# Kernel optimization log

Measured on AMD Instinct MI355X. Metric: run time of the kernel, lower is better.

The kernel has to match this reference:

```python
import jax, jax.numpy as jnp
import numpy as np

B, S, K, N = 4, 2048, 4096, 4096
GS = 128
G = K // GS  # 32 groups


def setup_inputs() -> dict:
    key = jax.random.key(0)
    k1, k2, k3, k4, k5 = jax.random.split(key, 5)
    x = jax.random.normal(k1, (B, S, K), dtype=jnp.float16)
    # packed 4-bit weights: 8 nibbles per int32 along K
    qweight = jax.random.randint(k2, (K // 8, N), 0, 2**31 - 1, dtype=jnp.int32)
    # packed 4-bit zeros: 8 nibbles per int32 along N
    qzeros = jax.random.randint(k3, (G, N // 8), 0, 2**31 - 1, dtype=jnp.int32)
    scales = (jax.random.uniform(k4, (G, N), dtype=jnp.float32) * 0.009 + 0.001).astype(jnp.float16)
    g_idx = (jnp.arange(K, dtype=jnp.int32) // GS).astype(jnp.int32)
    bias = (jax.random.normal(k5, (N,), dtype=jnp.float32) * 0.01).astype(jnp.float16)
    return {"x": x, "qweight": qweight, "qzeros": qzeros, "scales": scales,
            "g_idx": g_idx, "bias": bias}


def _dequantize(qweight, qzeros, scales, g_idx):
    """GPTQ/ExLlama int4 grouped dequant -> fp16 weight [K, N]."""
    shifts = jnp.arange(8, dtype=jnp.int32) * 4
    # unpack qweight along K: [K/8, N] -> [K/8, 8, N] -> [K, N]
    q = ((qweight[:, None, :] >> shifts[None, :, None]) & 0xF).reshape(-1, qweight.shape[1])
    # unpack qzeros along N: [G, N/8] -> [G, N/8, 8] -> [G, N]; GPTQ stores z-1
    z = (((qzeros[:, :, None] >> shifts[None, None, :]) & 0xF).reshape(qzeros.shape[0], -1) + 1)
    zr = z[g_idx]          # [K, N] via per-row group gather (act-order general form)
    sr = scales[g_idx]     # [K, N]
    return (q.astype(sr.dtype) - zr.astype(sr.dtype)) * sr


def reference(x, qweight, qzeros, scales, g_idx, bias):
    W = _dequantize(qweight, qzeros, scales, g_idx)  # [K, N] fp16
    xf = x.reshape(-1, x.shape[-1])                  # [B*S, K]
    out = jnp.matmul(xf, W, preferred_element_type=jnp.float32).astype(x.dtype)
    out = out.reshape(x.shape[:-1] + (W.shape[1],)) + bias
    return out
```

## Files before the change

### kernel.cpp

```cpp
#include <hip/hip_runtime.h>

typedef __attribute__((ext_vector_type(8))) _Float16 halfx8;
typedef __attribute__((ext_vector_type(8))) short short8;
typedef __attribute__((ext_vector_type(4))) float f32x4;

#define DI __device__ __forceinline__

DI unsigned short h2us(_Float16 h) { return __builtin_bit_cast(unsigned short, h); }

DI void gload_lds16(const void* g, void* l) {
  __builtin_amdgcn_global_load_lds(
      (const __attribute__((address_space(1))) void*)g,
      (__attribute__((address_space(3))) void*)l, 16, 0, 0);
}

__global__ void __launch_bounds__(256) conv_x(const float* __restrict__ x,
                                              unsigned short* __restrict__ Xh,
                                              long total) {
  long i = ((long)blockIdx.x * 256 + threadIdx.x) * 8;
  if (i >= total) return;
  f32x4 a = *(const f32x4*)&x[i];
  f32x4 b = *(const f32x4*)&x[i + 4];
  short8 v;
#pragma unroll
  for (int j = 0; j < 4; ++j) {
    v[j] = (short)h2us((_Float16)a[j]);
    v[4 + j] = (short)h2us((_Float16)b[j]);
  }
  *(short8*)&Xh[i] = v;
}

__global__ void __launch_bounds__(256) dequant_wt(
    const int* __restrict__ qweight, const int* __restrict__ qzeros,
    const float* __restrict__ scales, const int* __restrict__ g_idx,
    unsigned short* __restrict__ Wt, int N, int K) {
  int t = blockIdx.x * 256 + threadIdx.x;
  int n = t % N;
  int k0 = (t / N) * 64;
  if (k0 >= K) return;
  int g = g_idx[k0];
  float s = scales[(size_t)g * N + n];
  unsigned zw = (unsigned)qzeros[(size_t)g * (N >> 3) + (n >> 3)];
  int z1 = (int)((zw >> ((n & 7) * 4)) & 0xFu) + 1;
  int r0 = k0 >> 3;
#pragma unroll
  for (int i = 0; i < 8; ++i) {
    unsigned qw = (unsigned)qweight[(size_t)(r0 + i) * N + n];
    short8 v;
#pragma unroll
    for (int j = 0; j < 8; ++j) {
      int qi = (int)((qw >> (4 * j)) & 0xFu);
      v[j] = (short)h2us((_Float16)((float)(qi - z1) * s));
    }
    *(short8*)&Wt[(size_t)n * K + k0 + i * 8] = v;
  }
}

template <int MODE>
__global__ void __launch_bounds__(256, 2) gemm_f16(
    const unsigned short* __restrict__ Xh,
    const float* __restrict__ Xf,
    const unsigned short* __restrict__ Wt,
    const int* __restrict__ qweight, const int* __restrict__ qzeros,
    const float* __restrict__ scales, const int* __restrict__ g_idx,
    const float* __restrict__ bias, float* __restrict__ out,
    int M, int N, int K) {
  constexpr int BM = 128, BN = 128, BK = 32;
  __shared__ unsigned short Als[BM * BK];
  __shared__ unsigned short Bls[BN * BK];

  const int tid = threadIdx.x;
  const int lane = tid & 63;
  const int wave = tid >> 6;
  const int wr = wave >> 1, wc = wave & 1;
  const int nbm = M / BM;
  const int bm = blockIdx.x % nbm, bn = blockIdx.x / nbm;
  const int m0 = bm * BM, n0 = bn * BN;

  f32x4 acc[4][4] = {};

  const int lr = lane & 15;
  const int ko = (lane >> 4) * 8;

  for (int kk = 0; kk < K; kk += BK) {
    short8 av[2], bv[2];
    if constexpr (MODE != 0) {
#pragma unroll
      for (int i = 0; i < 2; ++i) {
        int e = i * 256 + tid;
        int row = e >> 2, uo = e & 3;
        const float* p = &Xf[(size_t)(m0 + row) * K + kk + uo * 8];
        f32x4 a = *(const f32x4*)p;
        f32x4 b = *(const f32x4*)(p + 4);
        short8 v;
#pragma unroll
        for (int j = 0; j < 4; ++j) {
          v[j] = (short)h2us((_Float16)a[j]);
          v[4 + j] = (short)h2us((_Float16)b[j]);
        }
        av[i] = v;
      }
    }
    if constexpr (MODE == 2) {
      int g = g_idx[kk];
      int r0k = kk >> 3;
#pragma unroll
      for (int i = 0; i < 2; ++i) {
        int w = i * 256 + tid;
        int n = n0 + (w >> 2);
        int r = r0k + (w & 3);
        unsigned qw = (unsigned)qweight[(size_t)r * N + n];
        float s = scales[(size_t)g * N + n];
        unsigned zw = (unsigned)qzeros[(size_t)g * (N >> 3) + (n >> 3)];
        int z1 = (int)((zw >> ((n & 7) * 4)) & 0xFu) + 1;
        short8 v;
#pragma unroll
        for (int j = 0; j < 8; ++j) {
          int qi = (int)((qw >> (4 * j)) & 0xFu);
          v[j] = (short)h2us((_Float16)((float)(qi - z1) * s));
        }
        bv[i] = v;
      }
    }

    __syncthreads();

    if constexpr (MODE == 0) {
#pragma unroll
      for (int i = 0; i < 2; ++i) {
        int e = i * 256 + tid;
        int row = e >> 2, uo = e & 3;
        gload_lds16(Xh + (size_t)(m0 + row) * K + kk + uo * 8, &Als[e * 8]);
        gload_lds16(Wt + (size_t)(n0 + row) * K + kk + uo * 8, &Bls[e * 8]);
      }
    } else {
      if constexpr (MODE == 1) {
#pragma unroll
        for (int i = 0; i < 2; ++i) {
          int e = i * 256 + tid;
          int row = e >> 2, uo = e & 3;
          gload_lds16(Wt + (size_t)(n0 + row) * K + kk + uo * 8, &Bls[e * 8]);
        }
      }
#pragma unroll
      for (int i = 0; i < 2; ++i) {
        int e = i * 256 + tid;
        *(short8*)&Als[e * 8] = av[i];
        if constexpr (MODE == 2) *(short8*)&Bls[e * 8] = bv[i];
      }
    }
    __syncthreads();

    halfx8 af[4], bfr[4];
#pragma unroll
    for (int mi = 0; mi < 4; ++mi)
      af[mi] = __builtin_bit_cast(
          halfx8, *(const short8*)&Als[(wr * 64 + mi * 16 + lr) * BK + ko]);
#pragma unroll
    for (int nj = 0; nj < 4; ++nj)
      bfr[nj] = __builtin_bit_cast(
          halfx8, *(const short8*)&Bls[(wc * 64 + nj * 16 + lr) * BK + ko]);
#pragma unroll
    for (int mi = 0; mi < 4; ++mi)
#pragma unroll
      for (int nj = 0; nj < 4; ++nj)
        acc[mi][nj] = __builtin_amdgcn_mfma_f32_16x16x32_f16(
            af[mi], bfr[nj], acc[mi][nj], 0, 0, 0);
  }

#pragma unroll
  for (int nj = 0; nj < 4; ++nj) {
    int col = n0 + wc * 64 + nj * 16 + lr;
    float bv2 = bias[col];
#pragma unroll
    for (int mi = 0; mi < 4; ++mi) {
      int row0 = m0 + wr * 64 + mi * 16 + ((lane >> 4) << 2);
#pragma unroll
      for (int j = 0; j < 4; ++j)
        out[(size_t)(row0 + j) * N + col] = acc[mi][nj][j] + bv2;
    }
  }
}

extern "C" void kernel_launch(void* const* d_in, const int* in_sizes, int n_in,
                              void* d_out, int out_size, void* d_ws,
                              size_t ws_size, hipStream_t stream) {
  const float* x = (const float*)d_in[0];
  const int* qweight = (const int*)d_in[1];
  const int* qzeros = (const int*)d_in[2];
  const float* scales = (const float*)d_in[3];
  const int* g_idx = (const int*)d_in[4];
  const float* bias = (const float*)d_in[5];
  float* out = (float*)d_out;

  const int K = in_sizes[4];
  const int N = in_sizes[5];
  const int M = in_sizes[0] / K;

  dim3 blk(256);
  dim3 grid((M / 128) * (N / 128));
  const size_t xh_bytes = (size_t)M * K * 2;
  const size_t wt_bytes = (size_t)N * K * 2;
  const long xtotal = (long)M * K;
  const int wt_blocks = (K / 64) * N / 256;

  if (ws_size >= xh_bytes + wt_bytes) {
    unsigned short* Xh = (unsigned short*)d_ws;
    unsigned short* Wt = (unsigned short*)((char*)d_ws + xh_bytes);
    conv_x<<<dim3((int)(xtotal / 2048)), blk, 0, stream>>>(x, Xh, xtotal);
    dequant_wt<<<dim3(wt_blocks), blk, 0, stream>>>(qweight, qzeros, scales,
                                                    g_idx, Wt, N, K);
    gemm_f16<0><<<grid, blk, 0, stream>>>(Xh, nullptr, Wt, qweight, qzeros,
                                          scales, g_idx, bias, out, M, N, K);
  } else if (ws_size >= wt_bytes) {
    unsigned short* Wt = (unsigned short*)d_ws;
    dequant_wt<<<dim3(wt_blocks), blk, 0, stream>>>(qweight, qzeros, scales,
                                                    g_idx, Wt, N, K);
    gemm_f16<1><<<grid, blk, 0, stream>>>(nullptr, x, Wt, qweight, qzeros,
                                          scales, g_idx, bias, out, M, N, K);
  } else {
    gemm_f16<2><<<grid, blk, 0, stream>>>(nullptr, x, nullptr, qweight, qzeros,
                                          scales, g_idx, bias, out, M, N, K);
  }
}
```

Measured before the change: 550.1 us.

## Replace GEMM with 256x256 tile, 4-stage async LDS pipeline and swizzle

Replaces the 128x128 single-buffered GEMM with a 512-thread 256x256-tile kernel. It uses a 4-deep ring of direct global-to-LDS loads with explicit vmcnt waits, an XOR-swizzled LDS layout to avoid bank conflicts, s_setprio around the MFMA block, and an XCD-aware block remap. The dequant kernel is reshaped so each thread writes one 16-byte chunk, giving coalesced-friendlier indexing. The fallback paths for small workspaces are dropped and 128 KB of dynamic LDS is requested, which assumes the workspace is large and limits occupancy.

```diff
diff --git a/kernel.cpp b/kernel.cpp
--- a/kernel.cpp
+++ b/kernel.cpp
@@ -34,150 +34,125 @@
     const int* __restrict__ qweight, const int* __restrict__ qzeros,
     const float* __restrict__ scales, const int* __restrict__ g_idx,
     unsigned short* __restrict__ Wt, int N, int K) {
-  int t = blockIdx.x * 256 + threadIdx.x;
-  int n = t % N;
-  int k0 = (t / N) * 64;
-  if (k0 >= K) return;
-  int g = g_idx[k0];
+  int T = blockIdx.x * 256 + threadIdx.x;
+  int oct = T & 7;
+  int rest = T >> 3;
+  int n = rest % N;
+  int kblk = rest / N;
+  int k = kblk * 64 + oct * 8;
+  if (k >= K) return;
+  int g = g_idx[k];
   float s = scales[(size_t)g * N + n];
   unsigned zw = (unsigned)qzeros[(size_t)g * (N >> 3) + (n >> 3)];
   int z1 = (int)((zw >> ((n & 7) * 4)) & 0xFu) + 1;
-  int r0 = k0 >> 3;
+  unsigned qw = (unsigned)qweight[(size_t)(kblk * 8 + oct) * N + n];
+  short8 v;
 #pragma unroll
-  for (int i = 0; i < 8; ++i) {
-    unsigned qw = (unsigned)qweight[(size_t)(r0 + i) * N + n];
-    short8 v;
-#pragma unroll
-    for (int j = 0; j < 8; ++j) {
-      int qi = (int)((qw >> (4 * j)) & 0xFu);
-      v[j] = (short)h2us((_Float16)((float)(qi - z1) * s));
-    }
-    *(short8*)&Wt[(size_t)n * K + k0 + i * 8] = v;
+  for (int j = 0; j < 8; ++j) {
+    int qi = (int)((qw >> (4 * j)) & 0xFu);
+    v[j] = (short)h2us((_Float16)((float)(qi - z1) * s));
   }
+  *(short8*)&Wt[(size_t)n * K + k] = v;
 }
 
-template <int MODE>
-__global__ void __launch_bounds__(256, 2) gemm_f16(
+__global__ void __launch_bounds__(512, 2) gemm256(
     const unsigned short* __restrict__ Xh,
-    const float* __restrict__ Xf,
     const unsigned short* __restrict__ Wt,
-    const int* __restrict__ qweight, const int* __restrict__ qzeros,
-    const float* __restrict__ scales, const int* __restrict__ g_idx,
     const float* __restrict__ bias, float* __restrict__ out,
     int M, int N, int K) {
-  constexpr int BM = 128, BN = 128, BK = 32;
-  __shared__ unsigned short Als[BM * BK];
-  __shared__ unsigned short Bls[BN * BK];
+  extern __shared__ unsigned short smem[];
+  unsigned short* As = smem;
+  unsigned short* Bs = smem + 4 * 8192;
 
   const int tid = threadIdx.x;
   const int lane = tid & 63;
   const int wave = tid >> 6;
-  const int wr = wave >> 1, wc = wave & 1;
-  const int nbm = M / BM;
-  const int bm = blockIdx.x % nbm, bn = blockIdx.x / nbm;
-  const int m0 = bm * BM, n0 = bn * BN;
+  const int wm = wave >> 2, wn = wave & 3;
 
-  f32x4 acc[4][4] = {};
+  const int cpx = gridDim.x >> 3;
+  const int wg = ((int)blockIdx.x & 7) * cpx + ((int)blockIdx.x >> 3);
+  const int nbm = M >> 8;
+  const int bm = wg % nbm, bn = wg / nbm;
+  const int m0 = bm << 8, n0 = bn << 8;
 
+  const int NT = K >> 5;
+
+  const int L0 = tid, L1 = 512 + tid;
+  const int r0s = L0 >> 2, c0 = (L0 & 3) ^ ((r0s >> 1) & 3);
+  const int r1s = L1 >> 2, c1 = (L1 & 3) ^ ((r1s >> 1) & 3);
+  const size_t aoff0 = (size_t)(m0 + r0s) * K + c0 * 8;
+  const size_t aoff1 = (size_t)(m0 + r1s) * K + c1 * 8;
+  const size_t boff0 = (size_t)(n0 + r0s) * K + c0 * 8;
+  const size_t boff1 = (size_t)(n0 + r1s) * K + c1 * 8;
+
+#define STAGE(t)                                               \
+  {                                                            \
+    int b_ = (t) & 3;                                          \
+    int kk_ = (t) << 5;                                        \
+    gload_lds16(Xh + aoff0 + kk_, &As[b_ * 8192 + L0 * 8]);    \
+    gload_lds16(Xh + aoff1 + kk_, &As[b_ * 8192 + L1 * 8]);    \
+    gload_lds16(Wt + boff0 + kk_, &Bs[b_ * 8192 + L0 * 8]);    \
+    gload_lds16(Wt + boff1 + kk_, &Bs[b_ * 8192 + L1 * 8]);    \
+  }
+
+  STAGE(0); STAGE(1); STAGE(2);
+  asm volatile("s_waitcnt vmcnt(8)" ::: "memory");
+  __builtin_amdgcn_s_barrier();
+  __builtin_amdgcn_sched_barrier(0);
+
+  f32x4 acc[8][4] = {};
   const int lr = lane & 15;
-  const int ko = (lane >> 4) * 8;
+  const int xch = (((lane >> 4) ^ ((lane >> 1) & 3)) * 8);
+  const int arow = wm * 128 + lr;
+  const int brow = wn * 64 + lr;
 
-  for (int kk = 0; kk < K; kk += BK) {
-    short8 av[2], bv[2];
-    if constexpr (MODE != 0) {
+  for (int t = 0; t < NT; ++t) {
+    if (t + 3 < NT) STAGE(t + 3);
+
+    const unsigned short* Ab = &As[(t & 3) * 8192];
+    const unsigned short* Bb = &Bs[(t & 3) * 8192];
+    halfx8 af[8], bf[4];
 #pragma unroll
-      for (int i = 0; i < 2; ++i) {
-        int e = i * 256 + tid;
-        int row = e >> 2, uo = e & 3;
-        const float* p = &Xf[(size_t)(m0 + row) * K + kk + uo * 8];
-        f32x4 a = *(const f32x4*)p;
-        f32x4 b = *(const f32x4*)(p + 4);
-        short8 v;
-#pragma unroll
-        for (int j = 0; j < 4; ++j) {
-          v[j] = (short)h2us((_Float16)a[j]);
-          v[4 + j] = (short)h2us((_Float16)b[j]);
-        }
-        av[i] = v;
-      }
-    }
-    if constexpr (MODE == 2) {
-      int g = g_idx[kk];
-      int r0k = kk >> 3;
-#pragma unroll
-      for (int i = 0; i < 2; ++i) {
-        int w = i * 256 + tid;
-        int n = n0 + (w >> 2);
-        int r = r0k + (w & 3);
-        unsigned qw = (unsigned)qweight[(size_t)r * N + n];
-        float s = scales[(size_t)g * N + n];
-        unsigned zw = (unsigned)qzeros[(size_t)g * (N >> 3) + (n >> 3)];
-        int z1 = (int)((zw >> ((n & 7) * 4)) & 0xFu) + 1;
-        short8 v;
-#pragma unroll
-        for (int j = 0; j < 8; ++j) {
-          int qi = (int)((qw >> (4 * j)) & 0xFu);
-          v[j] = (short)h2us((_Float16)((float)(qi - z1) * s));
-        }
-        bv[i] = v;
-      }
-    }
-
-    __syncthreads();
-
-    if constexpr (MODE == 0) {
-#pragma unroll
-      for (int i = 0; i < 2; ++i) {
-        int e = i * 256 + tid;
-        int row = e >> 2, uo = e & 3;
-        gload_lds16(Xh + (size_t)(m0 + row) * K + kk + uo * 8, &Als[e * 8]);
-        gload_lds16(Wt + (size_t)(n0 + row) * K + kk + uo * 8, &Bls[e * 8]);
-      }
-    } else {
-      if constexpr (MODE == 1) {
-#pragma unroll
-        for (int i = 0; i < 2; ++i) {
-          int e = i * 256 + tid;
-          int row = e >> 2, uo = e & 3;
-          gload_lds16(Wt + (size_t)(n0 + row) * K + kk + uo * 8, &Bls[e * 8]);
-        }
-      }
-#pragma unroll
-      for (int i = 0; i < 2; ++i) {
-        int e = i * 256 + tid;
-        *(short8*)&Als[e * 8] = av[i];
-        if constexpr (MODE == 2) *(short8*)&Bls[e * 8] = bv[i];
-      }
-    }
-    __syncthreads();
-
-    halfx8 af[4], bfr[4];
-#pragma unroll
-    for (int mi = 0; mi < 4; ++mi)
+    for (int mi = 0; mi < 8; ++mi)
       af[mi] = __builtin_bit_cast(
-          halfx8, *(const short8*)&Als[(wr * 64 + mi * 16 + lr) * BK + ko]);
+          halfx8, *(const short8*)&Ab[(arow + mi * 16) * 32 + xch]);
 #pragma unroll
     for (int nj = 0; nj < 4; ++nj)
-      bfr[nj] = __builtin_bit_cast(
-          halfx8, *(const short8*)&Bls[(wc * 64 + nj * 16 + lr) * BK + ko]);
+      bf[nj] = __builtin_bit_cast(
+          halfx8, *(const short8*)&Bb[(brow + nj * 16) * 32 + xch]);
+
+    __builtin_amdgcn_s_setprio(1);
 #pragma unroll
-    for (int mi = 0; mi < 4; ++mi)
+    for (int mi = 0; mi < 8; ++mi)
 #pragma unroll
       for (int nj = 0; nj < 4; ++nj)
         acc[mi][nj] = __builtin_amdgcn_mfma_f32_16x16x32_f16(
-            af[mi], bfr[nj], acc[mi][nj], 0, 0, 0);
+            af[mi], bf[nj], acc[mi][nj], 0, 0, 0);
+    __builtin_amdgcn_s_setprio(0);
+
+    if (t < NT - 3)
+      asm volatile("s_waitcnt vmcnt(8)" ::: "memory");
+    else if (t == NT - 3)
+      asm volatile("s_waitcnt vmcnt(4)" ::: "memory");
+    else
+      asm volatile("s_waitcnt vmcnt(0)" ::: "memory");
+    asm volatile("s_waitcnt lgkmcnt(0)" ::: "memory");
+    __builtin_amdgcn_sched_barrier(0);
+    __builtin_amdgcn_s_barrier();
+    __builtin_amdgcn_sched_barrier(0);
   }
+#undef STAGE
 
 #pragma unroll
   for (int nj = 0; nj < 4; ++nj) {
-    int col = n0 + wc * 64 + nj * 16 + lr;
-    float bv2 = bias[col];
+    int col = n0 + wn * 64 + nj * 16 + lr;
+    float bv = bias[col];
 #pragma unroll
-    for (int mi = 0; mi < 4; ++mi) {
-      int row0 = m0 + wr * 64 + mi * 16 + ((lane >> 4) << 2);
+    for (int mi = 0; mi < 8; ++mi) {
+      int row0 = m0 + wm * 128 + mi * 16 + ((lane >> 4) << 2);
 #pragma unroll
       for (int j = 0; j < 4; ++j)
-        out[(size_t)(row0 + j) * N + col] = acc[mi][nj][j] + bv2;
+        out[(size_t)(row0 + j) * N + col] = acc[mi][nj][j] + bv;
     }
   }
 }
@@ -197,29 +172,19 @@
   const int N = in_sizes[5];
   const int M = in_sizes[0] / K;
 
-  dim3 blk(256);
-  dim3 grid((M / 128) * (N / 128));
-  const size_t xh_bytes = (size_t)M * K * 2;
-  const size_t wt_bytes = (size_t)N * K * 2;
+  unsigned short* Xh = (unsigned short*)d_ws;
+  unsigned short* Wtp = (unsigned short*)((char*)d_ws + (size_t)M * K * 2);
+
   const long xtotal = (long)M * K;
-  const int wt_blocks = (K / 64) * N / 256;
+  conv_x<<<dim3((int)(xtotal / 2048)), dim3(256), 0, stream>>>(x, Xh, xtotal);
 
-  if (ws_size >= xh_bytes + wt_bytes) {
-    unsigned short* Xh = (unsigned short*)d_ws;
-    unsigned short* Wt = (unsigned short*)((char*)d_ws + xh_bytes);
-    conv_x<<<dim3((int)(xtotal / 2048)), blk, 0, stream>>>(x, Xh, xtotal);
-    dequant_wt<<<dim3(wt_blocks), blk, 0, stream>>>(qweight, qzeros, scales,
-                                                    g_idx, Wt, N, K);
-    gemm_f16<0><<<grid, blk, 0, stream>>>(Xh, nullptr, Wt, qweight, qzeros,
-                                          scales, g_idx, bias, out, M, N, K);
-  } else if (ws_size >= wt_bytes) {
-    unsigned short* Wt = (unsigned short*)d_ws;
-    dequant_wt<<<dim3(wt_blocks), blk, 0, stream>>>(qweight, qzeros, scales,
-                                                    g_idx, Wt, N, K);
-    gemm_f16<1><<<grid, blk, 0, stream>>>(nullptr, x, Wt, qweight, qzeros,
-                                          scales, g_idx, bias, out, M, N, K);
-  } else {
-    gemm_f16<2><<<grid, blk, 0, stream>>>(nullptr, x, nullptr, qweight, qzeros,
-                                          scales, g_idx, bias, out, M, N, K);
-  }
+  const int dq_blocks = (int)(((size_t)N * (K / 8)) / 256);
+  dequant_wt<<<dim3(dq_blocks), dim3(256), 0, stream>>>(qweight, qzeros,
+                                                        scales, g_idx, Wtp, N, K);
+
+  const int grid = (M / 256) * (N / 256);
+  hipFuncSetAttribute((const void*)gemm256,
+                      hipFuncAttributeMaxDynamicSharedMemorySize, 131072);
+  gemm256<<<dim3(grid), dim3(512), 131072, stream>>>(Xh, Wtp, bias, out,
+                                                     M, N, K);
 }
```

After: 503.4 us. 8.5% less time.
